# Performance work log

Measured on AMD Instinct MI355X. Metric: run time of the kernel, lower is better.

The kernel has to match this reference:

```python
import jax, jax.numpy as jnp
import numpy as np

N_EMBD = 1024
N_HEAD = 16

def setup_inputs() -> dict:
    key = jax.random.key(0)
    ks = jax.random.split(key, 5)
    s = 0.02
    return {
        "x": jax.random.normal(ks[0], (4, 2048, N_EMBD), dtype=jnp.float32),
        "w_attn": jax.random.normal(ks[1], (N_EMBD, 3 * N_EMBD), dtype=jnp.float32) * s,
        "b_attn": jnp.zeros((3 * N_EMBD,), dtype=jnp.float32),
        "w_proj": jax.random.normal(ks[2], (N_EMBD, N_EMBD), dtype=jnp.float32) * s,
        "b_proj": jnp.zeros((N_EMBD,), dtype=jnp.float32),
    }

def reference(x, w_attn, b_attn, w_proj, b_proj):
    B, T, C = x.shape
    H = N_HEAD
    D = C // H
    qkv = x @ w_attn + b_attn                       # [B,T,3C]
    q, k, v = jnp.split(qkv, 3, axis=-1)
    # [B,H,T,D]
    q = q.reshape(B, T, H, D).transpose(0, 2, 1, 3)
    k = k.reshape(B, T, H, D).transpose(0, 2, 1, 3)
    v = v.reshape(B, T, H, D).transpose(0, 2, 1, 3)
    scale = 1.0 / jnp.sqrt(jnp.asarray(D, dtype=x.dtype))
    attn = jnp.einsum("bhqd,bhkd->bhqk", q, k) * scale
    mask = jnp.tril(jnp.ones((T, T), dtype=bool))
    attn = jnp.where(mask, attn, jnp.asarray(-jnp.inf, dtype=attn.dtype))
    attn = jax.nn.softmax(attn, axis=-1)
    out = jnp.einsum("bhqk,bhkd->bhqd", attn, v)    # [B,H,T,D]
    out = out.transpose(0, 2, 1, 3).reshape(B, T, C)
    return out @ w_proj + b_proj
```

## Files before the change

### kernel.cpp

```cpp
#include <hip/hip_runtime.h>


typedef unsigned short u16b;
typedef __bf16 bf16x8 __attribute__((ext_vector_type(8)));
typedef float f32x4 __attribute__((ext_vector_type(4)));
typedef float f32x16 __attribute__((ext_vector_type(16)));
typedef unsigned short u16x4 __attribute__((ext_vector_type(4)));

#define AS1(p) ((const __attribute__((address_space(1))) void*)(p))
#define AS3(p) ((__attribute__((address_space(3))) void*)(p))
#define GLDS(g, l) __builtin_amdgcn_global_load_lds(AS1(g), AS3(l), 16, 0, 0)

__device__ __forceinline__ u16b bfr(float v) {
  union { float f; unsigned u; } x; x.f = v;
  unsigned r = x.u + 0x7fffu + ((x.u >> 16) & 1u);
  return (u16b)(r >> 16);
}

__device__ __forceinline__ unsigned pk2(float lo, float hi) {
  union { __bf16 h[2]; unsigned u; } t;
  t.h[0] = (__bf16)lo; t.h[1] = (__bf16)hi;
  return t.u;
}

__device__ __forceinline__ float max16(const f32x16& v) {
  float a0 = fmaxf(v[0], v[1]), a1 = fmaxf(v[2], v[3]);
  float a2 = fmaxf(v[4], v[5]), a3 = fmaxf(v[6], v[7]);
  float b0 = fmaxf(v[8], v[9]), b1 = fmaxf(v[10], v[11]);
  float b2 = fmaxf(v[12], v[13]), b3 = fmaxf(v[14], v[15]);
  float c0 = fmaxf(a0, a1), c1 = fmaxf(a2, a3);
  float c2 = fmaxf(b0, b1), c3 = fmaxf(b2, b3);
  return fmaxf(fmaxf(c0, c1), fmaxf(c2, c3));
}

__device__ __forceinline__ float sum16(const f32x16& v) {
  float a0 = v[0] + v[1], a1 = v[2] + v[3], a2 = v[4] + v[5], a3 = v[6] + v[7];
  float b0 = v[8] + v[9], b1 = v[10] + v[11], b2 = v[12] + v[13], b3 = v[14] + v[15];
  float c0 = a0 + a1, c1 = a2 + a3, c2 = b0 + b1, c3 = b2 + b3;
  return (c0 + c1) + (c2 + c3);
}

__global__ __launch_bounds__(256) void cvt_bf16_kernel(
    const float* __restrict__ src, u16b* __restrict__ dst, int n4) {
  int i = blockIdx.x * 256 + threadIdx.x;
  const int stride = gridDim.x * 256;
  for (; i < n4; i += stride) {
    const float4 v = reinterpret_cast<const float4*>(src)[i];
    u16x4 o;
    o[0] = bfr(v.x); o[1] = bfr(v.y); o[2] = bfr(v.z); o[3] = bfr(v.w);
    reinterpret_cast<u16x4*>(dst)[i] = o;
  }
}

__global__ __launch_bounds__(256) void transpose_cvt_kernel(
    const float* __restrict__ src, u16b* __restrict__ dst, int R, int C) {
  __shared__ u16b tile[64][72];
  const int nc = C >> 6;
  const int br = blockIdx.x / nc, bc = blockIdx.x % nc;
  const int r0 = br << 6, c0 = bc << 6;
  const int c = threadIdx.x & 63, r4 = threadIdx.x >> 6;
  #pragma unroll
  for (int i = 0; i < 16; ++i) {
    const int r = r4 + 4 * i;
    tile[r][c] = bfr(src[(size_t)(r0 + r) * C + c0 + c]);
  }
  __syncthreads();
  #pragma unroll
  for (int i = 0; i < 16; ++i) {
    const int rr = r4 + 4 * i;
    dst[(size_t)(c0 + rr) * R + r0 + c] = tile[c][rr];
  }
}

template <int EPI>
__global__ __launch_bounds__(256, 2) void gemm128_kernel(
    const u16b* __restrict__ A, const u16b* __restrict__ Bt,
    const float* __restrict__ bias,
    u16b* __restrict__ oQ, u16b* __restrict__ oK, u16b* __restrict__ oVt,
    float* __restrict__ oF, int M, int N, int K) {
  __shared__ u16b smem[16384];
  const int tid = threadIdx.x;
  const int wid = tid >> 6, lane = tid & 63;
  const int nb = N >> 7;
  const int lin = (blockIdx.x & 7) * ((int)gridDim.x >> 3) + (blockIdx.x >> 3);
  const int brow = lin / nb, bcol = lin % nb;
  const int wr = (wid >> 1) << 6, wc = (wid & 1) << 6;

  f32x4 acc[4][4] = {};

  const int ar = (wid << 4) + (lane >> 2);
  const int ac = (lane & 3) << 3;
  const u16b* Ab = A + (size_t)((brow << 7) + ar) * K + ac;
  const u16b* Bb = Bt + (size_t)((bcol << 7) + ar) * K + ac;
  const int fr = lane & 15;
  const int fk = (lane >> 4) << 3;
  const int nk = K >> 5;

#define STAGE(bufi, kk)                                                        \
  {                                                                            \
    char* sb = (char*)smem + (bufi) * 16384;                                   \
    GLDS(Ab + (kk),                  sb + wid * 1024);                         \
    GLDS(Ab + (size_t)64 * K + (kk), sb + 4096 + wid * 1024);                  \
    GLDS(Bb + (kk),                  sb + 8192 + wid * 1024);                  \
    GLDS(Bb + (size_t)64 * K + (kk), sb + 12288 + wid * 1024);                 \
  }

  STAGE(0, 0);
  STAGE(1, 32);

  #pragma unroll 1
  for (int kt = 0; kt < nk; ++kt) {
    if (kt + 1 < nk) asm volatile("s_waitcnt vmcnt(4)" ::: "memory");
    else             asm volatile("s_waitcnt vmcnt(0)" ::: "memory");
    __builtin_amdgcn_s_barrier();

    const u16b* As = (const u16b*)((const char*)smem + (kt & 1) * 16384);
    const u16b* Bs = As + 4096;
    bf16x8 af[4], bfv[4];
    #pragma unroll
    for (int i = 0; i < 4; ++i)
      af[i] = *(const bf16x8*)&As[(wr + i * 16 + fr) * 32 + fk];
    #pragma unroll
    for (int j = 0; j < 4; ++j)
      bfv[j] = *(const bf16x8*)&Bs[(wc + j * 16 + fr) * 32 + fk];
    __builtin_amdgcn_s_setprio(1);
    #pragma unroll
    for (int i = 0; i < 4; ++i)
      #pragma unroll
      for (int j = 0; j < 4; ++j)
        acc[i][j] = __builtin_amdgcn_mfma_f32_16x16x32_bf16(af[i], bfv[j], acc[i][j], 0, 0, 0);
    __builtin_amdgcn_s_setprio(0);

    __builtin_amdgcn_s_barrier();
    if (kt + 2 < nk) STAGE(kt & 1, (kt + 2) << 5);
  }
#undef STAGE

  const int fq = lane >> 4;
  if (EPI == 1) {
    #pragma unroll
    for (int j = 0; j < 4; ++j) {
      const int n0 = (bcol << 7) + wc + j * 16 + fr;
      const float bv = bias[n0];
      #pragma unroll
      for (int i = 0; i < 4; ++i) {
        #pragma unroll
        for (int r = 0; r < 4; ++r) {
          const int m0 = (brow << 7) + wr + i * 16 + fq * 4 + r;
          oF[(size_t)m0 * N + n0] = acc[i][j][r] + bv;
        }
      }
    }
  } else {
    const int sect = bcol >> 3;
    if (sect < 2) {
      const float qs = (sect == 0) ? 0.1803368801f : 1.0f;
      u16b* oPtr = (sect == 0) ? oQ : oK;
      u16b* tile = (u16b*)smem;
      #pragma unroll
      for (int j = 0; j < 4; ++j) {
        const int n = wc + j * 16 + fr;
        const float bv = bias[(bcol << 7) + n];
        #pragma unroll
        for (int i = 0; i < 4; ++i) {
          #pragma unroll
          for (int r = 0; r < 4; ++r) {
            const int m = wr + i * 16 + fq * 4 + r;
            const int byteoff = m * 256 + (((n >> 3) ^ (m & 7)) << 4) + ((n & 7) << 1);
            *(u16b*)((char*)tile + byteoff) = bfr((acc[i][j][r] + bv) * qs);
          }
        }
      }
      __syncthreads();
      const int nh = wid >> 1;
      const int c = lane & 7;
      #pragma unroll
      for (int it = 0; it < 8; ++it) {
        const int m = ((wid & 1) << 6) + (it << 3) + (lane >> 3);
        const int chunk = (nh << 3) + (c ^ (m & 7));
        const bf16x8 val = *(const bf16x8*)((const char*)tile + m * 256 + chunk * 16);
        const int m0 = (brow << 7) + m;
        const int n0 = (bcol << 7) + (nh << 6) + (c << 3);
        const int bb = m0 >> 11, tt = m0 & 2047;
        const int h = (n0 >> 6) & 15, d = n0 & 63;
        *(bf16x8*)(oPtr + (((size_t)(bb * 16 + h) * 2048 + tt) * 64 + d)) = val;
      }
    } else {
      u16b* tile = (u16b*)smem;
      #pragma unroll
      for (int j = 0; j < 4; ++j) {
        const int nl = wc + j * 16 + fr;
        const float bv = bias[(bcol << 7) + nl];
        #pragma unroll
        for (int i = 0; i < 4; ++i) {
          #pragma unroll
          for (int r = 0; r < 4; ++r) {
            const int m = wr + i * 16 + fq * 4 + r;
            const int byteoff = nl * 256 + (((m >> 3) ^ (nl & 7)) << 4) + ((m & 7) << 1);
            *(u16b*)((char*)tile + byteoff) = bfr(acc[i][j][r] + bv);
          }
        }
      }
      __syncthreads();
      const int row0 = wid << 5;
      const int c16 = lane & 15;
      const int rr = lane >> 4;
      const int t0 = (brow << 7) & 2047;
      const int bb = brow >> 4;
      #pragma unroll
      for (int it = 0; it < 8; ++it) {
        const int nl = row0 + (it << 2) + rr;
        const int pch = c16 ^ (nl & 7);
        const bf16x8 val = *(const bf16x8*)((const char*)tile + nl * 256 + pch * 16);
        const int h = ((bcol & 7) << 1) + (nl >> 6);
        const int d = nl & 63;
        *(bf16x8*)(oVt + ((size_t)((bb << 4) + h) * 64 + d) * 2048 + t0 + (c16 << 3)) = val;
      }
    }
  }
}

__global__ __launch_bounds__(256, 2) void flash_kernel(
    const u16b* __restrict__ Q, const u16b* __restrict__ K,
    const u16b* __restrict__ Vt, u16b* __restrict__ O) {
  __shared__ u16b smem[32768];
  const int bid = blockIdx.x;
  const int bh = bid & 63;
  const int dp = bid >> 6;
  const int p = (dp < 4) ? dp : (11 - dp);
  const int g1 = p, g2 = 15 - p;
  const int tid = threadIdx.x, wid = tid >> 6, lane = tid & 63;
  const int ln31 = lane & 31, hi = lane >> 5;
  const int l7 = ln31 & 7;
  const size_t baseQK = (size_t)bh * 2048 * 64;
  const size_t baseV = (size_t)bh * 64 * 2048;
  const int b = bh >> 4, h = bh & 15;
  const int rk = lane >> 3;
  const int sk = ((lane & 7) ^ rk) << 3;
  const int rv = lane >> 4;
  const int cv = lane & 15;

#define FSTAGE(kt, bi)                                                         \
  {                                                                            \
    char* kb_ = (char*)smem + (bi) * 32768;                                    \
    char* vb_ = kb_ + 16384;                                                   \
    const int k0_ = (kt) << 7;                                                 \
    _Pragma("unroll")                                                          \
    for (int c = 0; c < 4; ++c) {                                              \
      const int i = 4 * wid + c;                                               \
      const int r = 8 * i + rk;                                                \
      GLDS(K + baseQK + (size_t)(k0_ + r) * 64 + sk, kb_ + i * 1024);          \
    }                                                                          \
    _Pragma("unroll")                                                          \
    for (int c = 0; c < 4; ++c) {                                              \
      const int i = 4 * wid + c;                                               \
      const int r = 4 * i + rv;                                                \
      const int scv = (cv ^ (r & 7)) << 3;                                     \
      GLDS(Vt + baseV + (size_t)r * 2048 + k0_ + scv, vb_ + i * 1024);         \
    }                                                                          \
  }

  const int q0wA = (g1 << 7) + wid * 32;
  const int q0wB = (g2 << 7) + wid * 32;

  bf16x8 qfA[4], qfB[4];
  {
    const u16b* qpA = Q + baseQK + (size_t)(q0wA + ln31) * 64 + hi * 8;
    const u16b* qpB = Q + baseQK + (size_t)(q0wB + ln31) * 64 + hi * 8;
    #pragma unroll
    for (int kk = 0; kk < 4; ++kk) {
      qfA[kk] = *(const bf16x8*)(qpA + kk * 16);
      qfB[kk] = *(const bf16x8*)(qpB + kk * 16);
    }
  }

  float mA = -3e38f, lA = 0.f, mB = -3e38f, lB = 0.f;
  f32x16 oaA0 = {}, oaA1 = {}, oaB0 = {}, oaB1 = {};

  FSTAGE(0, 0);
  FSTAGE(1, 1);

  #pragma unroll 1
  for (int kt = 0; kt <= g2; ++kt) {
    if (kt < g2) asm volatile("s_waitcnt vmcnt(8)" ::: "memory");
    else         asm volatile("s_waitcnt vmcnt(0)" ::: "memory");
    __builtin_amdgcn_s_barrier();

    const char* kb = (const char*)smem + (kt & 1) * 32768;
    const char* vb = kb + 16384;

    auto compute_tile = [&](const bf16x8* qf, float& m_run, float& l_run,
                            f32x16& oa0, f32x16& oa1, const int gq) {
      const bool diag = (kt == gq);
      const int maxsub = diag ? wid : 3;

      f32x16 s[4] = {};
      __builtin_amdgcn_s_setprio(1);
      #pragma unroll
      for (int ss = 0; ss < 4; ++ss) {
        if (ss <= maxsub) {
          const int row = 32 * ss + ln31;
          #pragma unroll
          for (int kk = 0; kk < 4; ++kk) {
            const int ch = (2 * kk + hi) ^ l7;
            const bf16x8 kf = *(const bf16x8*)(kb + row * 128 + ch * 16);
            s[ss] = __builtin_amdgcn_mfma_f32_32x32x16_bf16(kf, qf[kk], s[ss], 0, 0, 0);
          }
        }
      }
      __builtin_amdgcn_s_setprio(0);

      if (diag) {
        #pragma unroll
        for (int ss = 0; ss < 4; ++ss) {
          if (ss == wid) {
            #pragma unroll
            for (int r = 0; r < 16; ++r) {
              const int kvr = (r & 3) + 8 * (r >> 2) + 4 * hi;
              if (kvr > ln31) s[ss][r] = -3e38f;
            }
          }
        }
      }

      float tm = -3e38f;
      #pragma unroll
      for (int ss = 0; ss < 4; ++ss)
        if (ss <= maxsub) tm = fmaxf(tm, max16(s[ss]));
      tm = fmaxf(tm, __shfl_xor(tm, 32));

      if (!__all(tm <= m_run + 8.f)) {
        const float mnew = fmaxf(m_run, tm);
        const float scale = __builtin_amdgcn_exp2f(m_run - mnew);
        m_run = mnew;
        l_run *= scale;
        #pragma unroll
        for (int r = 0; r < 16; ++r) { oa0[r] *= scale; oa1[r] *= scale; }
      }

      float rs = 0.f;
      #pragma unroll
      for (int ss = 0; ss < 4; ++ss) {
        if (ss <= maxsub) {
          #pragma unroll
          for (int r = 0; r < 16; ++r)
            s[ss][r] = __builtin_amdgcn_exp2f(s[ss][r] - m_run);
          rs += sum16(s[ss]);
        }
      }
      rs += __shfl_xor(rs, 32);
      l_run += rs;

      union WB { unsigned u[4]; bf16x8 v; };
      __builtin_amdgcn_s_setprio(1);
      #pragma unroll
      for (int ss = 0; ss < 4; ++ss) {
        if (ss <= maxsub) {
          WB pA, pB;
#define MKPA(W0, W1, W2, W3, P0, P1, P2, P3, P4, P5, P6, P7)                 \
          {                                                                   \
            unsigned a0 = pk2(P0, P1), a1 = pk2(P2, P3);                      \
            unsigned b0 = pk2(P4, P5), b1 = pk2(P6, P7);                      \
            auto r0 = __builtin_amdgcn_permlane32_swap(a0, b0, false, false); \
            auto r1 = __builtin_amdgcn_permlane32_swap(a1, b1, false, false); \
            unsigned o0[2], o1[2];                                            \
            __builtin_memcpy(o0, &r0, 8); __builtin_memcpy(o1, &r1, 8);       \
            W0 = o0[0]; W2 = o0[1]; W1 = o1[0]; W3 = o1[1];                   \
          }
          MKPA(pA.u[0], pA.u[1], pA.u[2], pA.u[3],
               s[ss][0], s[ss][1], s[ss][2], s[ss][3],
               s[ss][4], s[ss][5], s[ss][6], s[ss][7]);
          MKPA(pB.u[0], pB.u[1], pB.u[2], pB.u[3],
               s[ss][8], s[ss][9], s[ss][10], s[ss][11],
               s[ss][12], s[ss][13], s[ss][14], s[ss][15]);
#undef MKPA
          const int cxa = ((4 * ss + hi) ^ l7) << 4;
          const int cxb = ((4 * ss + 2 + hi) ^ l7) << 4;
          const char* v0 = vb + ln31 * 256;
          const char* v1 = vb + (32 + ln31) * 256;
          oa0 = __builtin_amdgcn_mfma_f32_32x32x16_bf16(*(const bf16x8*)(v0 + cxa), pA.v, oa0, 0, 0, 0);
          oa1 = __builtin_amdgcn_mfma_f32_32x32x16_bf16(*(const bf16x8*)(v1 + cxa), pA.v, oa1, 0, 0, 0);
          oa0 = __builtin_amdgcn_mfma_f32_32x32x16_bf16(*(const bf16x8*)(v0 + cxb), pB.v, oa0, 0, 0, 0);
          oa1 = __builtin_amdgcn_mfma_f32_32x32x16_bf16(*(const bf16x8*)(v1 + cxb), pB.v, oa1, 0, 0, 0);
        }
      }
      __builtin_amdgcn_s_setprio(0);
    };

    compute_tile(qfB, mB, lB, oaB0, oaB1, g2);
    if (kt <= g1) compute_tile(qfA, mA, lA, oaA0, oaA1, g1);

    __builtin_amdgcn_s_barrier();
    if (kt + 2 <= g2) FSTAGE(kt + 2, kt & 1);
  }

  {
    const float inv = 1.0f / lA;
    const int q = q0wA + ln31;
    u16b* orow = O + (size_t)(b * 2048 + q) * 1024 + h * 64;
    #pragma unroll
    for (int rq = 0; rq < 4; ++rq) {
      u16x4 v0, v1;
      #pragma unroll
      for (int j = 0; j < 4; ++j) {
        v0[j] = bfr(oaA0[4 * rq + j] * inv);
        v1[j] = bfr(oaA1[4 * rq + j] * inv);
      }
      const int d0 = 8 * rq + 4 * hi;
      *(u16x4*)(orow + d0) = v0;
      *(u16x4*)(orow + 32 + d0) = v1;
    }
  }
  {
    const float inv = 1.0f / lB;
    const int q = q0wB + ln31;
    u16b* orow = O + (size_t)(b * 2048 + q) * 1024 + h * 64;
    #pragma unroll
    for (int rq = 0; rq < 4; ++rq) {
      u16x4 v0, v1;
      #pragma unroll
      for (int j = 0; j < 4; ++j) {
        v0[j] = bfr(oaB0[4 * rq + j] * inv);
        v1[j] = bfr(oaB1[4 * rq + j] * inv);
      }
      const int d0 = 8 * rq + 4 * hi;
      *(u16x4*)(orow + d0) = v0;
      *(u16x4*)(orow + 32 + d0) = v1;
    }
  }
#undef FSTAGE
}

extern "C" void kernel_launch(void* const* d_in, const int* in_sizes, int n_in,
                              void* d_out, int out_size, void* d_ws, size_t ws_size,
                              hipStream_t stream) {
  const float* x      = (const float*)d_in[0];
  const float* w_attn = (const float*)d_in[1];
  const float* b_attn = (const float*)d_in[2];
  const float* w_proj = (const float*)d_in[3];
  const float* b_proj = (const float*)d_in[4];
  float* out = (float*)d_out;
  char* ws = (char*)d_ws;

  u16b* xb  = (u16b*)(ws + 0);
  u16b* waT = (u16b*)(ws + 16777216);
  u16b* wpT = (u16b*)(ws + 23068672);
  u16b* Qb  = (u16b*)(ws + 25165824);
  u16b* Kb  = (u16b*)(ws + 41943040);
  u16b* Vtb = (u16b*)(ws + 75497472);
  u16b* attn = xb;

  cvt_bf16_kernel<<<2048, 256, 0, stream>>>(x, xb, (8192 * 1024) / 4);
  transpose_cvt_kernel<<<16 * 48, 256, 0, stream>>>(w_attn, waT, 1024, 3072);
  transpose_cvt_kernel<<<16 * 16, 256, 0, stream>>>(w_proj, wpT, 1024, 1024);
  gemm128_kernel<0><<<64 * 24, 256, 0, stream>>>(xb, waT, b_attn, Qb, Kb, Vtb, nullptr,
                                                 8192, 3072, 1024);
  flash_kernel<<<512, 256, 0, stream>>>(Qb, Kb, Vtb, attn);
  gemm128_kernel<1><<<64 * 8, 256, 0, stream>>>(attn, wpT, b_proj, nullptr, nullptr, nullptr,
                                                out, 8192, 1024, 1024);
}
```

Measured before the change: 171.9 us.

## Swizzle GEMM LDS layout and share K fragments across both query tiles

The GEMM kernel now XOR-swizzles the 16-byte column chunks both in its global-to-LDS staging addresses and in its fragment reads, to reduce LDS bank conflicts. In the attention loop, when both query tiles are active, each K fragment is loaded from LDS once and fed to the MFMAs for both tiles. The softmax and PV stages of the two tiles are then interleaved, which gives the scheduler more independent work. In exchange, two score tiles (sA and sB) are live at the same time, which raises register pressure and could lower occupancy or cause spills.

```diff
diff --git a/kernel.cpp b/kernel.cpp
--- a/kernel.cpp
+++ b/kernel.cpp
@@ -21,6 +21,20 @@
   union { __bf16 h[2]; unsigned u; } t;
   t.h[0] = (__bf16)lo; t.h[1] = (__bf16)hi;
   return t.u;
+}
+
+union WB { unsigned u[4]; bf16x8 v; };
+
+template <int O>
+__device__ __forceinline__ WB packh(const f32x16& s) {
+  unsigned a0 = pk2(s[O + 0], s[O + 1]), a1 = pk2(s[O + 2], s[O + 3]);
+  unsigned b0 = pk2(s[O + 4], s[O + 5]), b1 = pk2(s[O + 6], s[O + 7]);
+  auto r0 = __builtin_amdgcn_permlane32_swap(a0, b0, false, false);
+  auto r1 = __builtin_amdgcn_permlane32_swap(a1, b1, false, false);
+  unsigned o0[2], o1[2];
+  __builtin_memcpy(o0, &r0, 8); __builtin_memcpy(o1, &r1, 8);
+  WB w; w.u[0] = o0[0]; w.u[2] = o0[1]; w.u[1] = o1[0]; w.u[3] = o1[1];
+  return w;
 }
 
 __device__ __forceinline__ float max16(const f32x16& v) {
@@ -89,11 +103,11 @@
   f32x4 acc[4][4] = {};
 
   const int ar = (wid << 4) + (lane >> 2);
-  const int ac = (lane & 3) << 3;
-  const u16b* Ab = A + (size_t)((brow << 7) + ar) * K + ac;
-  const u16b* Bb = Bt + (size_t)((bcol << 7) + ar) * K + ac;
+  const int acs = (((lane & 3) ^ ((lane >> 3) & 3))) << 3;
+  const u16b* Ab = A + (size_t)((brow << 7) + ar) * K + acs;
+  const u16b* Bb = Bt + (size_t)((bcol << 7) + ar) * K + acs;
   const int fr = lane & 15;
-  const int fk = (lane >> 4) << 3;
+  const int pcs = (((lane >> 4) ^ ((fr >> 1) & 3))) << 4;
   const int nk = K >> 5;
 
 #define STAGE(bufi, kk)                                                        \
@@ -114,15 +128,15 @@
     else             asm volatile("s_waitcnt vmcnt(0)" ::: "memory");
     __builtin_amdgcn_s_barrier();
 
-    const u16b* As = (const u16b*)((const char*)smem + (kt & 1) * 16384);
-    const u16b* Bs = As + 4096;
+    const char* As = (const char*)smem + (kt & 1) * 16384;
+    const char* Bs = As + 8192;
     bf16x8 af[4], bfv[4];
     #pragma unroll
     for (int i = 0; i < 4; ++i)
-      af[i] = *(const bf16x8*)&As[(wr + i * 16 + fr) * 32 + fk];
+      af[i] = *(const bf16x8*)(As + (wr + i * 16 + fr) * 64 + pcs);
     #pragma unroll
     for (int j = 0; j < 4; ++j)
-      bfv[j] = *(const bf16x8*)&Bs[(wc + j * 16 + fr) * 32 + fk];
+      bfv[j] = *(const bf16x8*)(Bs + (wc + j * 16 + fr) * 64 + pcs);
     __builtin_amdgcn_s_setprio(1);
     #pragma unroll
     for (int i = 0; i < 4; ++i)
@@ -280,6 +294,69 @@
   FSTAGE(0, 0);
   FSTAGE(1, 1);
 
+  auto mask_diag = [&](f32x16* s) {
+    #pragma unroll
+    for (int ss = 0; ss < 4; ++ss) {
+      if (ss == wid) {
+        #pragma unroll
+        for (int r = 0; r < 16; ++r) {
+          const int kvr = (r & 3) + 8 * (r >> 2) + 4 * hi;
+          if (kvr > ln31) s[ss][r] = -3e38f;
+        }
+      }
+    }
+  };
+
+  auto softmax_tile = [&](f32x16* s, float& m_run, float& l_run,
+                          f32x16& oa0, f32x16& oa1, const int maxsub) {
+    float tm = -3e38f;
+    #pragma unroll
+    for (int ss = 0; ss < 4; ++ss)
+      if (ss <= maxsub) tm = fmaxf(tm, max16(s[ss]));
+    tm = fmaxf(tm, __shfl_xor(tm, 32));
+    if (!__all(tm <= m_run + 8.f)) {
+      const float mnew = fmaxf(m_run, tm);
+      const float scale = __builtin_amdgcn_exp2f(m_run - mnew);
+      m_run = mnew;
+      l_run *= scale;
+      #pragma unroll
+      for (int r = 0; r < 16; ++r) { oa0[r] *= scale; oa1[r] *= scale; }
+    }
+    float rs = 0.f;
+    #pragma unroll
+    for (int ss = 0; ss < 4; ++ss) {
+      if (ss <= maxsub) {
+        #pragma unroll
+        for (int r = 0; r < 16; ++r)
+          s[ss][r] = __builtin_amdgcn_exp2f(s[ss][r] - m_run);
+        rs += sum16(s[ss]);
+      }
+    }
+    rs += __shfl_xor(rs, 32);
+    l_run += rs;
+  };
+
+  auto pv_tile = [&](f32x16* s, f32x16& oa0, f32x16& oa1,
+                     const int maxsub, const char* vb) {
+    __builtin_amdgcn_s_setprio(1);
+    #pragma unroll
+    for (int ss = 0; ss < 4; ++ss) {
+      if (ss <= maxsub) {
+        const WB pa = packh<0>(s[ss]);
+        const WB pb = packh<8>(s[ss]);
+        const int cxa = ((4 * ss + hi) ^ l7) << 4;
+        const int cxb = ((4 * ss + 2 + hi) ^ l7) << 4;
+        const char* v0 = vb + ln31 * 256;
+        const char* v1 = vb + (32 + ln31) * 256;
+        oa0 = __builtin_amdgcn_mfma_f32_32x32x16_bf16(*(const bf16x8*)(v0 + cxa), pa.v, oa0, 0, 0, 0);
+        oa1 = __builtin_amdgcn_mfma_f32_32x32x16_bf16(*(const bf16x8*)(v1 + cxa), pa.v, oa1, 0, 0, 0);
+        oa0 = __builtin_amdgcn_mfma_f32_32x32x16_bf16(*(const bf16x8*)(v0 + cxb), pb.v, oa0, 0, 0, 0);
+        oa1 = __builtin_amdgcn_mfma_f32_32x32x16_bf16(*(const bf16x8*)(v1 + cxb), pb.v, oa1, 0, 0, 0);
+      }
+    }
+    __builtin_amdgcn_s_setprio(0);
+  };
+
   #pragma unroll 1
   for (int kt = 0; kt <= g2; ++kt) {
     if (kt < g2) asm volatile("s_waitcnt vmcnt(8)" ::: "memory");
@@ -289,106 +366,54 @@
     const char* kb = (const char*)smem + (kt & 1) * 32768;
     const char* vb = kb + 16384;
 
-    auto compute_tile = [&](const bf16x8* qf, float& m_run, float& l_run,
-                            f32x16& oa0, f32x16& oa1, const int gq) {
-      const bool diag = (kt == gq);
-      const int maxsub = diag ? wid : 3;
-
-      f32x16 s[4] = {};
+    if (kt <= g1) {
+      const int maxA = (kt == g1) ? wid : 3;
+      f32x16 sB[4] = {}, sA[4] = {};
       __builtin_amdgcn_s_setprio(1);
       #pragma unroll
       for (int ss = 0; ss < 4; ++ss) {
-        if (ss <= maxsub) {
+        const int row = 32 * ss + ln31;
+        bf16x8 kf[4];
+        #pragma unroll
+        for (int kk = 0; kk < 4; ++kk)
+          kf[kk] = *(const bf16x8*)(kb + row * 128 + (((2 * kk + hi) ^ l7) << 4));
+        #pragma unroll
+        for (int kk = 0; kk < 4; ++kk)
+          sB[ss] = __builtin_amdgcn_mfma_f32_32x32x16_bf16(kf[kk], qfB[kk], sB[ss], 0, 0, 0);
+        if (ss <= maxA) {
+          #pragma unroll
+          for (int kk = 0; kk < 4; ++kk)
+            sA[ss] = __builtin_amdgcn_mfma_f32_32x32x16_bf16(kf[kk], qfA[kk], sA[ss], 0, 0, 0);
+        }
+      }
+      __builtin_amdgcn_s_setprio(0);
+
+      if (kt == g1) mask_diag(sA);
+      softmax_tile(sB, mB, lB, oaB0, oaB1, 3);
+      softmax_tile(sA, mA, lA, oaA0, oaA1, maxA);
+      pv_tile(sB, oaB0, oaB1, 3, vb);
+      pv_tile(sA, oaA0, oaA1, maxA, vb);
+    } else {
+      const int maxB = (kt == g2) ? wid : 3;
+      f32x16 sB[4] = {};
+      __builtin_amdgcn_s_setprio(1);
+      #pragma unroll
+      for (int ss = 0; ss < 4; ++ss) {
+        if (ss <= maxB) {
           const int row = 32 * ss + ln31;
           #pragma unroll
           for (int kk = 0; kk < 4; ++kk) {
-            const int ch = (2 * kk + hi) ^ l7;
-            const bf16x8 kf = *(const bf16x8*)(kb + row * 128 + ch * 16);
-            s[ss] = __builtin_amdgcn_mfma_f32_32x32x16_bf16(kf, qf[kk], s[ss], 0, 0, 0);
+            const bf16x8 kf = *(const bf16x8*)(kb + row * 128 + (((2 * kk + hi) ^ l7) << 4));
+            sB[ss] = __builtin_amdgcn_mfma_f32_32x32x16_bf16(kf, qfB[kk], sB[ss], 0, 0, 0);
           }
         }
       }
       __builtin_amdgcn_s_setprio(0);
 
-      if (diag) {
-        #pragma unroll
-        for (int ss = 0; ss < 4; ++ss) {
-          if (ss == wid) {
-            #pragma unroll
-            for (int r = 0; r < 16; ++r) {
-              const int kvr = (r & 3) + 8 * (r >> 2) + 4 * hi;
-              if (kvr > ln31) s[ss][r] = -3e38f;
-            }
-          }
-        }
-      }
-
-      float tm = -3e38f;
-      #pragma unroll
-      for (int ss = 0; ss < 4; ++ss)
-        if (ss <= maxsub) tm = fmaxf(tm, max16(s[ss]));
-      tm = fmaxf(tm, __shfl_xor(tm, 32));
-
-      if (!__all(tm <= m_run + 8.f)) {
-        const float mnew = fmaxf(m_run, tm);
-        const float scale = __builtin_amdgcn_exp2f(m_run - mnew);
-        m_run = mnew;
-        l_run *= scale;
-        #pragma unroll
-        for (int r = 0; r < 16; ++r) { oa0[r] *= scale; oa1[r] *= scale; }
-      }
-
-      float rs = 0.f;
-      #pragma unroll
-      for (int ss = 0; ss < 4; ++ss) {
-        if (ss <= maxsub) {
-          #pragma unroll
-          for (int r = 0; r < 16; ++r)
-            s[ss][r] = __builtin_amdgcn_exp2f(s[ss][r] - m_run);
-          rs += sum16(s[ss]);
-        }
-      }
-      rs += __shfl_xor(rs, 32);
-      l_run += rs;
-
-      union WB { unsigned u[4]; bf16x8 v; };
-      __builtin_amdgcn_s_setprio(1);
-      #pragma unroll
-      for (int ss = 0; ss < 4; ++ss) {
-        if (ss <= maxsub) {
-          WB pA, pB;
-#define MKPA(W0, W1, W2, W3, P0, P1, P2, P3, P4, P5, P6, P7)                 \
-          {                                                                   \
-            unsigned a0 = pk2(P0, P1), a1 = pk2(P2, P3);                      \
-            unsigned b0 = pk2(P4, P5), b1 = pk2(P6, P7);                      \
-            auto r0 = __builtin_amdgcn_permlane32_swap(a0, b0, false, false); \
-            auto r1 = __builtin_amdgcn_permlane32_swap(a1, b1, false, false); \
-            unsigned o0[2], o1[2];                                            \
-            __builtin_memcpy(o0, &r0, 8); __builtin_memcpy(o1, &r1, 8);       \
-            W0 = o0[0]; W2 = o0[1]; W1 = o1[0]; W3 = o1[1];                   \
-          }
-          MKPA(pA.u[0], pA.u[1], pA.u[2], pA.u[3],
-               s[ss][0], s[ss][1], s[ss][2], s[ss][3],
-               s[ss][4], s[ss][5], s[ss][6], s[ss][7]);
-          MKPA(pB.u[0], pB.u[1], pB.u[2], pB.u[3],
-               s[ss][8], s[ss][9], s[ss][10], s[ss][11],
-               s[ss][12], s[ss][13], s[ss][14], s[ss][15]);
-#undef MKPA
-          const int cxa = ((4 * ss + hi) ^ l7) << 4;
-          const int cxb = ((4 * ss + 2 + hi) ^ l7) << 4;
-          const char* v0 = vb + ln31 * 256;
-          const char* v1 = vb + (32 + ln31) * 256;
-          oa0 = __builtin_amdgcn_mfma_f32_32x32x16_bf16(*(const bf16x8*)(v0 + cxa), pA.v, oa0, 0, 0, 0);
-          oa1 = __builtin_amdgcn_mfma_f32_32x32x16_bf16(*(const bf16x8*)(v1 + cxa), pA.v, oa1, 0, 0, 0);
-          oa0 = __builtin_amdgcn_mfma_f32_32x32x16_bf16(*(const bf16x8*)(v0 + cxb), pB.v, oa0, 0, 0, 0);
-          oa1 = __builtin_amdgcn_mfma_f32_32x32x16_bf16(*(const bf16x8*)(v1 + cxb), pB.v, oa1, 0, 0, 0);
-        }
-      }
-      __builtin_amdgcn_s_setprio(0);
-    };
-
-    compute_tile(qfB, mB, lB, oaB0, oaB1, g2);
-    if (kt <= g1) compute_tile(qfA, mA, lA, oaA0, oaA1, g1);
+      if (kt == g2) mask_diag(sB);
+      softmax_tile(sB, mB, lB, oaB0, oaB1, maxB);
+      pv_tile(sB, oaB0, oaB1, maxB, vb);
+    }
 
     __builtin_amdgcn_s_barrier();
     if (kt + 2 <= g2) FSTAGE(kt + 2, kt & 1);
```

Result: slower. 302.6 us (+76.0%).
